# Kernel tuning notes

Measured on AMD Instinct MI355X. Metric: run time of the kernel, lower is better.

The kernel has to match this reference:

```python
import jax, jax.numpy as jnp
import numpy as np

C = 768
N = 2048
BS = 8
MASK_VAL = 1e10


def _sincos(n, c):
    # torch sinusoidal_position_embedding: interleaved sin/cos, then
    # cos_pos = emb[..., 1::2].repeat_interleave(2), sin_pos = emb[..., ::2].repeat_interleave(2)
    pos = jnp.arange(n, dtype=jnp.float32)[:, None]            # [N,1]
    inv = jnp.power(10000.0, -2.0 * jnp.arange(c // 2, dtype=jnp.float32) / c)  # [C/2]
    ang = pos * inv                                            # [N, C/2]
    sin = jnp.repeat(jnp.sin(ang), 2, axis=-1)                 # [N, C]
    cos = jnp.repeat(jnp.cos(ang), 2, axis=-1)                 # [N, C]
    return sin[None], cos[None]                                # [1, N, C]


def _rope(x, sin, cos):
    # x2 = interleave(-x_odd, x_even)
    x2 = jnp.stack([-x[..., 1::2], x[..., ::2]], axis=-1).reshape(x.shape)
    return x * cos + x2 * sin


def _global_pointer(x, Wq, bq, Wk, bk, sin, cos, mask):
    xq = jnp.einsum('bnc,dc->bnd', x, Wq) + bq
    xk = jnp.einsum('bnc,dc->bnd', x, Wk) + bk
    xq = _rope(xq, sin, cos)
    xk = _rope(xk, sin, cos)
    logits = jnp.einsum('bnd,bmd->bnm', xq, xk)
    logits = logits - mask * MASK_VAL
    return logits / jnp.sqrt(jnp.float32(C))


def setup_inputs() -> dict:
    key = jax.random.key(0)
    ks = jax.random.split(key, 9)
    s = 0.02
    return {
        'feature': jax.random.normal(ks[0], (BS, N, C), jnp.float32),
        'Wq': jax.random.normal(ks[1], (C, C), jnp.float32) * s,
        'bq': jax.random.normal(ks[2], (C,), jnp.float32) * s,
        'Wk': jax.random.normal(ks[3], (C, C), jnp.float32) * s,
        'bk': jax.random.normal(ks[4], (C,), jnp.float32) * s,
        'Wq_cls': jax.random.normal(ks[5], (C, C), jnp.float32) * s,
        'bq_cls': jax.random.normal(ks[6], (C,), jnp.float32) * s,
        'Wk_cls': jax.random.normal(ks[7], (C, C), jnp.float32) * s,
        'bk_cls': jax.random.normal(ks[8], (C,), jnp.float32) * s,
    }


def reference(feature, Wq, bq, Wk, bk, Wq_cls, bq_cls, Wk_cls, bk_cls):
    n = feature.shape[1]
    sin, cos = _sincos(n, C)
    mask = jnp.tril(jnp.ones((n, n), jnp.float32), k=-1)  # strictly lower triangular
    gp = _global_pointer(feature, Wq, bq, Wk, bk, sin, cos, mask)
    gp_cls = _global_pointer(feature, Wq_cls, bq_cls, Wk_cls, bk_cls, sin, cos, mask)
    # stacked: [2, bs, N, N] = (global_pointer, global_pointer_cls)
    return jnp.stack([gp, gp_cls], axis=0)
```

## Files before the change

### kernel.cpp

```cpp
#include <hip/hip_runtime.h>
#include <hip/hip_bf16.h>
#include <stdint.h>

typedef unsigned short u16;
typedef __attribute__((ext_vector_type(8))) __bf16 bf16x8;
typedef __attribute__((ext_vector_type(4))) float f32x4;

#define C_DIM 768
#define HALF_C 384
#define N_SEQ 2048
#define BATCH 8
#define M_TOT (BATCH * N_SEQ)
#define BK 32
#define NT (C_DIM / BK)

__device__ __forceinline__ u16 f2bf(float f) {
    union { float f; unsigned u; } c; c.f = f;
    unsigned r = (c.u + 0x7FFFu + ((c.u >> 16) & 1u)) >> 16;
    return (u16)r;
}

#define PREP_XBLK 12288
#define PREP_WBLK 576
#define PREP_SBLK 3072
__global__ __launch_bounds__(256) void prep_kernel(
    const float* __restrict__ feat,
    const float* __restrict__ Wq, const float* __restrict__ Wk,
    const float* __restrict__ Wqc, const float* __restrict__ Wkc,
    u16* __restrict__ xbf,
    u16* __restrict__ w0, u16* __restrict__ w1,
    u16* __restrict__ w2, u16* __restrict__ w3,
    uint32_t* __restrict__ cs_tab) {
    const int b = blockIdx.x, tid = threadIdx.x;
    if (b < PREP_XBLK + 4 * PREP_WBLK) {
        const float* src; u16* dst; int base;
        if (b < PREP_XBLK)                    { src = feat; dst = xbf; base = 0; }
        else if (b < PREP_XBLK + PREP_WBLK)   { src = Wq;  dst = w0; base = PREP_XBLK; }
        else if (b < PREP_XBLK + 2*PREP_WBLK) { src = Wk;  dst = w1; base = PREP_XBLK + PREP_WBLK; }
        else if (b < PREP_XBLK + 3*PREP_WBLK) { src = Wqc; dst = w2; base = PREP_XBLK + 2*PREP_WBLK; }
        else                                  { src = Wkc; dst = w3; base = PREP_XBLK + 3*PREP_WBLK; }
        const int i = (b - base) * 256 + tid;
        float4 v = ((const float4*)src)[i];
        ushort4 o;
        o.x = f2bf(v.x); o.y = f2bf(v.y); o.z = f2bf(v.z); o.w = f2bf(v.w);
        ((ushort4*)dst)[i] = o;
    } else {
        const int idx = (b - PREP_XBLK - 4 * PREP_WBLK) * 256 + tid;
        const int pos = idx / HALF_C;
        const int ip  = idx - pos * HALF_C;
        float inv = powf(10000.0f, (-2.0f / (float)C_DIM) * (float)ip);
        float ang = (float)pos * inv;
        uint32_t c = f2bf(cosf(ang)), s = f2bf(sinf(ang));
        cs_tab[idx] = (s << 16) | c;
    }
}

template<int N> __device__ __forceinline__ void vmwait();
template<> __device__ __forceinline__ void vmwait<8>() { asm volatile("s_waitcnt vmcnt(8)" ::: "memory"); }
template<> __device__ __forceinline__ void vmwait<4>() { asm volatile("s_waitcnt vmcnt(4)" ::: "memory"); }
template<> __device__ __forceinline__ void vmwait<0>() { asm volatile("s_waitcnt vmcnt(0)" ::: "memory"); }

__device__ __forceinline__ void async_load16(const void* src, void* dst_lds) {
    const __attribute__((address_space(1))) void* g =
        (const __attribute__((address_space(1))) void*)(uintptr_t)src;
    __attribute__((address_space(3))) void* l =
        (__attribute__((address_space(3))) void*)(unsigned)(uintptr_t)dst_lds;
    __builtin_amdgcn_global_load_lds(g, l, 16, 0, 0);
}

__device__ __forceinline__ void stage32(const u16* __restrict__ gbase, int ld,
                                        u16* ldsbase, int wave, int lane) {
    const int s  = (lane & 3) ^ ((lane >> 4) & 3);
    const int rr = lane >> 2;
    #pragma unroll
    for (int j = 0; j < 2; ++j) {
        const int chunk = wave * 2 + j;
        const u16* src = gbase + (size_t)(chunk * 16 + rr) * ld + s * 8;
        u16* dst = ldsbase + chunk * 512;
        async_load16(src, dst);
    }
}

__device__ __forceinline__ void gemm256_mainloop(
    const u16* __restrict__ A, const u16* __restrict__ B, int ld,
    u16* LdsA, u16* LdsB, f32x4 (&acc)[8][4], int wave, int lane) {

    #pragma unroll
    for (int t = 0; t < 3; ++t) {
        stage32(A + t * BK, ld, LdsA + t * 8192, wave, lane);
        stage32(B + t * BK, ld, LdsB + t * 8192, wave, lane);
    }
    __builtin_amdgcn_sched_barrier(0);
    vmwait<8>();
    __builtin_amdgcn_s_barrier();
    __builtin_amdgcn_sched_barrier(0);

    const int r = lane & 15, sl = lane >> 4;
    const int lane_off = r * 32 + ((sl ^ ((r >> 2) & 3)) * 8);
    const int wm = wave >> 2, wn = wave & 3;
    const int a_base = lane_off + wm * 512;
    const int b_base = lane_off + wn * 512;

    #pragma unroll
    for (int t = 0; t < NT; ++t) {
        const u16* At = LdsA + (t & 3) * 8192;
        const u16* Bt = LdsB + (t & 3) * 8192;
        bf16x8 a[4], b[4], a2[4];

        if (t + 3 < NT) stage32(A + (t + 3) * BK, ld, LdsA + ((t + 3) & 3) * 8192, wave, lane);
        #pragma unroll
        for (int mf = 0; mf < 4; ++mf) a[mf] = *(const bf16x8*)(At + a_base + mf * 1024);
        #pragma unroll
        for (int nf = 0; nf < 4; ++nf) b[nf] = *(const bf16x8*)(Bt + b_base + nf * 2048);
        __builtin_amdgcn_sched_barrier(0);
        __builtin_amdgcn_s_barrier();
        __builtin_amdgcn_sched_barrier(0);
        __builtin_amdgcn_s_setprio(1);
        #pragma unroll
        for (int mf = 0; mf < 4; ++mf)
            #pragma unroll
            for (int nf = 0; nf < 4; ++nf)
                acc[mf][nf] = __builtin_amdgcn_mfma_f32_16x16x32_bf16(a[mf], b[nf], acc[mf][nf], 0, 0, 0);
        __builtin_amdgcn_s_setprio(0);
        __builtin_amdgcn_sched_barrier(0);
        __builtin_amdgcn_s_barrier();
        __builtin_amdgcn_sched_barrier(0);

        if (t + 3 < NT) stage32(B + (t + 3) * BK, ld, LdsB + ((t + 3) & 3) * 8192, wave, lane);
        #pragma unroll
        for (int mf = 0; mf < 4; ++mf) a2[mf] = *(const bf16x8*)(At + a_base + (mf + 4) * 1024);
        __builtin_amdgcn_sched_barrier(0);
        __builtin_amdgcn_s_barrier();
        __builtin_amdgcn_sched_barrier(0);
        __builtin_amdgcn_s_setprio(1);
        #pragma unroll
        for (int mf = 0; mf < 4; ++mf)
            #pragma unroll
            for (int nf = 0; nf < 4; ++nf)
                acc[mf + 4][nf] = __builtin_amdgcn_mfma_f32_16x16x32_bf16(a2[mf], b[nf], acc[mf + 4][nf], 0, 0, 0);
        __builtin_amdgcn_s_setprio(0);
        __builtin_amdgcn_sched_barrier(0);
        if (t <= NT - 4)      vmwait<8>();
        else if (t == NT - 3) vmwait<4>();
        else if (t == NT - 2) vmwait<0>();
        __builtin_amdgcn_s_barrier();
        __builtin_amdgcn_sched_barrier(0);
    }
}

__global__ __launch_bounds__(512, 2) void proj_kernel(
    const u16* __restrict__ xbf,
    const u16* __restrict__ W0, const u16* __restrict__ W1,
    const u16* __restrict__ W2, const u16* __restrict__ W3,
    const float* __restrict__ b0, const float* __restrict__ b1,
    const float* __restrict__ b2, const float* __restrict__ b3,
    u16* __restrict__ o0, u16* __restrict__ o1, u16* __restrict__ o2, u16* __restrict__ o3,
    const uint32_t* __restrict__ cs_tab) {
    __shared__ __align__(16) u16 LdsA[4 * 8192];
    __shared__ __align__(16) u16 LdsB[4 * 8192];
    const int tid = threadIdx.x, lane = tid & 63, wave = tid >> 6;
    const int bid = blockIdx.x;
    const int swz = (bid & 7) * 96 + (bid >> 3);
    const int z   = swz / 192;
    const int rem = swz % 192;
    const int by  = rem / 64;
    const int bx  = rem % 64;
    const int m0 = bx * 256, n0 = by * 256;

    const u16*   W    = z == 0 ? W0 : z == 1 ? W1 : z == 2 ? W2 : W3;
    const float* bias = z == 0 ? b0 : z == 1 ? b1 : z == 2 ? b2 : b3;
    u16*         outp = z == 0 ? o0 : z == 1 ? o1 : z == 2 ? o2 : o3;

    f32x4 acc[8][4];
    #pragma unroll
    for (int x = 0; x < 8; ++x)
        #pragma unroll
        for (int y = 0; y < 4; ++y) acc[x][y] = f32x4{0.f, 0.f, 0.f, 0.f};

    gemm256_mainloop(xbf + (size_t)m0 * C_DIM, W + (size_t)n0 * C_DIM, C_DIM,
                     LdsA, LdsB, acc, wave, lane);

    const int wm = wave >> 2, wn = wave & 3;
    const int g = lane >> 4, r = lane & 15;
    #pragma unroll
    for (int nf = 0; nf < 4; ++nf) {
        const int col = n0 + nf * 64 + wn * 16 + r;
        const float bv = bias[col];
        const int ip = col >> 1;
        const float sgn = (col & 1) ? 1.0f : -1.0f;
        #pragma unroll
        for (int mf = 0; mf < 8; ++mf) {
            #pragma unroll
            for (int i = 0; i < 4; ++i) {
                const int row = m0 + mf * 32 + wm * 16 + g * 4 + i;
                const int pos = row & (N_SEQ - 1);
                float v = acc[mf][nf][i] + bv;
                float p = __shfl_xor(v, 1);
                const uint32_t cs = cs_tab[pos * HALF_C + ip];
                const float c = __uint_as_float(cs << 16);
                const float s = __uint_as_float(cs & 0xFFFF0000u);
                outp[(size_t)row * C_DIM + col] = f2bf(v * c + sgn * p * s);
            }
        }
    }
}

__global__ __launch_bounds__(512, 2) void logits_kernel(
    const u16* __restrict__ Q0, const u16* __restrict__ K0,
    const u16* __restrict__ Q1, const u16* __restrict__ K1,
    float* __restrict__ out) {
    __shared__ __align__(16) u16 LdsA[4 * 8192];
    __shared__ __align__(16) u16 LdsB[4 * 8192];
    const int tid = threadIdx.x, lane = tid & 63, wave = tid >> 6;
    const int bid = blockIdx.x;
    const int swz = (bid & 7) * 128 + (bid >> 3);
    const int z   = swz >> 6;
    const int rem = swz & 63;
    const int by  = rem >> 3;
    const int bx  = rem & 7;
    const int nrow0 = by * 256, mcol0 = bx * 256;

    const float RS = 0.036084391824351613f;
    const float MV = 1.0e10f * RS;
    float* outz = out + (size_t)z * N_SEQ * N_SEQ;

    if (bx < by) {
        const float4 cv = {-MV, -MV, -MV, -MV};
        #pragma unroll
        for (int i = 0; i < 32; ++i) {
            const int row = nrow0 + wave * 32 + i;
            *(float4*)(outz + (size_t)row * N_SEQ + mcol0 + lane * 4) = cv;
        }
        return;
    }

    const int h = z >> 3, b = z & 7;
    const u16* Qb = (h ? Q1 : Q0) + (size_t)b * N_SEQ * C_DIM;
    const u16* Kb = (h ? K1 : K0) + (size_t)b * N_SEQ * C_DIM;

    f32x4 acc[8][4];
    #pragma unroll
    for (int x = 0; x < 8; ++x)
        #pragma unroll
        for (int y = 0; y < 4; ++y) acc[x][y] = f32x4{0.f, 0.f, 0.f, 0.f};

    gemm256_mainloop(Qb + (size_t)nrow0 * C_DIM, Kb + (size_t)mcol0 * C_DIM, C_DIM,
                     LdsA, LdsB, acc, wave, lane);

    const int wm = wave >> 2, wn = wave & 3;
    const int g = lane >> 4, r = lane & 15;
    #pragma unroll
    for (int mf = 0; mf < 8; ++mf) {
        #pragma unroll
        for (int i = 0; i < 4; ++i) {
            const int row = nrow0 + mf * 32 + wm * 16 + g * 4 + i;
            float* orow = outz + (size_t)row * N_SEQ;
            #pragma unroll
            for (int nf = 0; nf < 4; ++nf) {
                const int col = mcol0 + nf * 64 + wn * 16 + r;
                orow[col] = acc[mf][nf][i] * RS - (col < row ? MV : 0.0f);
            }
        }
    }
}

extern "C" void kernel_launch(void* const* d_in, const int* in_sizes, int n_in,
                              void* d_out, int out_size, void* d_ws, size_t ws_size,
                              hipStream_t stream) {
    (void)in_sizes; (void)n_in; (void)out_size; (void)ws_size;
    const float* feat = (const float*)d_in[0];
    const float* Wq   = (const float*)d_in[1];
    const float* bq   = (const float*)d_in[2];
    const float* Wk   = (const float*)d_in[3];
    const float* bk   = (const float*)d_in[4];
    const float* Wqc  = (const float*)d_in[5];
    const float* bqc  = (const float*)d_in[6];
    const float* Wkc  = (const float*)d_in[7];
    const float* bkc  = (const float*)d_in[8];
    float* out = (float*)d_out;

    u16* ws = (u16*)d_ws;
    const size_t XE = (size_t)M_TOT * C_DIM;
    const size_t WE = (size_t)C_DIM * C_DIM;
    u16* xbf = ws;
    u16* Wb0 = ws + XE;
    u16* Wb1 = Wb0 + WE;
    u16* Wb2 = Wb1 + WE;
    u16* Wb3 = Wb2 + WE;
    u16* qkbase = Wb3 + WE;
    u16* Qa = qkbase;
    u16* Ka = qkbase + XE;
    u16* Qc = qkbase + 2 * XE;
    u16* Kc = qkbase + 3 * XE;
    uint32_t* cs_tab = (uint32_t*)(qkbase + 4 * XE);

    prep_kernel<<<dim3(PREP_XBLK + 4 * PREP_WBLK + PREP_SBLK), dim3(256), 0, stream>>>(
        feat, Wq, Wk, Wqc, Wkc, xbf, Wb0, Wb1, Wb2, Wb3, cs_tab);

    proj_kernel<<<dim3(768), dim3(512), 0, stream>>>(
        xbf, Wb0, Wb1, Wb2, Wb3, bq, bk, bqc, bkc, Qa, Ka, Qc, Kc, cs_tab);

    logits_kernel<<<dim3(1024), dim3(512), 0, stream>>>(
        Qa, Ka, Qc, Kc, out);
}
```

Baseline: 219.6 us.

## Shrink GEMM tiles to 128x256 with triple-buffered LDS and higher occupancy

Both GEMM kernels move from 256x256 tiles with a 4-stage split A/B LDS buffer to 128x256 tiles with a unified 3-stage buffer, and the per-iteration loop drops from two MFMA phases to one. Launch bounds rise to 4 blocks per CU and grid sizes double. The aim is more resident waves for latency hiding and finer-grained triangle skipping in the logits kernel. In exchange, each tile reuses operands less, the prefetch depth is shallower, and global traffic for the B operand goes up.

```diff
diff --git a/kernel.cpp b/kernel.cpp
--- a/kernel.cpp
+++ b/kernel.cpp
@@ -56,8 +56,7 @@
 }
 
 template<int N> __device__ __forceinline__ void vmwait();
-template<> __device__ __forceinline__ void vmwait<8>() { asm volatile("s_waitcnt vmcnt(8)" ::: "memory"); }
-template<> __device__ __forceinline__ void vmwait<4>() { asm volatile("s_waitcnt vmcnt(4)" ::: "memory"); }
+template<> __device__ __forceinline__ void vmwait<3>() { asm volatile("s_waitcnt vmcnt(3)" ::: "memory"); }
 template<> __device__ __forceinline__ void vmwait<0>() { asm volatile("s_waitcnt vmcnt(0)" ::: "memory"); }
 
 __device__ __forceinline__ void async_load16(const void* src, void* dst_lds) {
@@ -68,50 +67,51 @@
     __builtin_amdgcn_global_load_lds(g, l, 16, 0, 0);
 }
 
-__device__ __forceinline__ void stage32(const u16* __restrict__ gbase, int ld,
-                                        u16* ldsbase, int wave, int lane) {
+template<int NROWS>
+__device__ __forceinline__ void stageT(const u16* __restrict__ g, int ld,
+                                       u16* ldsbase, int wave, int lane) {
     const int s  = (lane & 3) ^ ((lane >> 4) & 3);
     const int rr = lane >> 2;
     #pragma unroll
-    for (int j = 0; j < 2; ++j) {
-        const int chunk = wave * 2 + j;
-        const u16* src = gbase + (size_t)(chunk * 16 + rr) * ld + s * 8;
-        u16* dst = ldsbase + chunk * 512;
-        async_load16(src, dst);
-    }
-}
-
-__device__ __forceinline__ void gemm256_mainloop(
+    for (int j = 0; j < NROWS / 128; ++j) {
+        const int chunk = wave + j * 8;
+        const u16* src = g + (size_t)(chunk * 16 + rr) * ld + s * 8;
+        async_load16(src, ldsbase + chunk * 512);
+    }
+}
+
+__device__ __forceinline__ void gemm_mainloop(
     const u16* __restrict__ A, const u16* __restrict__ B, int ld,
-    u16* LdsA, u16* LdsB, f32x4 (&acc)[8][4], int wave, int lane) {
-
-    #pragma unroll
-    for (int t = 0; t < 3; ++t) {
-        stage32(A + t * BK, ld, LdsA + t * 8192, wave, lane);
-        stage32(B + t * BK, ld, LdsB + t * 8192, wave, lane);
-    }
+    u16* Lds, f32x4 (&acc)[4][4], int wave, int lane) {
+
+    stageT<128>(A, ld, Lds, wave, lane);
+    stageT<256>(B, ld, Lds + 4096, wave, lane);
+    stageT<128>(A + BK, ld, Lds + 12288, wave, lane);
+    stageT<256>(B + BK, ld, Lds + 12288 + 4096, wave, lane);
     __builtin_amdgcn_sched_barrier(0);
-    vmwait<8>();
+    vmwait<3>();
     __builtin_amdgcn_s_barrier();
     __builtin_amdgcn_sched_barrier(0);
 
     const int r = lane & 15, sl = lane >> 4;
     const int lane_off = r * 32 + ((sl ^ ((r >> 2) & 3)) * 8);
     const int wm = wave >> 2, wn = wave & 3;
-    const int a_base = lane_off + wm * 512;
-    const int b_base = lane_off + wn * 512;
+    const int a_base = lane_off + wm * 2048;
+    const int b_base = 4096 + lane_off + wn * 2048;
 
     #pragma unroll
     for (int t = 0; t < NT; ++t) {
-        const u16* At = LdsA + (t & 3) * 8192;
-        const u16* Bt = LdsB + (t & 3) * 8192;
-        bf16x8 a[4], b[4], a2[4];
-
-        if (t + 3 < NT) stage32(A + (t + 3) * BK, ld, LdsA + ((t + 3) & 3) * 8192, wave, lane);
-        #pragma unroll
-        for (int mf = 0; mf < 4; ++mf) a[mf] = *(const bf16x8*)(At + a_base + mf * 1024);
-        #pragma unroll
-        for (int nf = 0; nf < 4; ++nf) b[nf] = *(const bf16x8*)(Bt + b_base + nf * 2048);
+        const u16* S = Lds + (t % 3) * 12288;
+        if (t + 2 < NT) {
+            u16* D = Lds + ((t + 2) % 3) * 12288;
+            stageT<128>(A + (t + 2) * BK, ld, D, wave, lane);
+            stageT<256>(B + (t + 2) * BK, ld, D + 4096, wave, lane);
+        }
+        bf16x8 a[4], b[4];
+        #pragma unroll
+        for (int mf = 0; mf < 4; ++mf) a[mf] = *(const bf16x8*)(S + a_base + mf * 512);
+        #pragma unroll
+        for (int nf = 0; nf < 4; ++nf) b[nf] = *(const bf16x8*)(S + b_base + nf * 512);
         __builtin_amdgcn_sched_barrier(0);
         __builtin_amdgcn_s_barrier();
         __builtin_amdgcn_sched_barrier(0);
@@ -123,32 +123,14 @@
                 acc[mf][nf] = __builtin_amdgcn_mfma_f32_16x16x32_bf16(a[mf], b[nf], acc[mf][nf], 0, 0, 0);
         __builtin_amdgcn_s_setprio(0);
         __builtin_amdgcn_sched_barrier(0);
-        __builtin_amdgcn_s_barrier();
-        __builtin_amdgcn_sched_barrier(0);
-
-        if (t + 3 < NT) stage32(B + (t + 3) * BK, ld, LdsB + ((t + 3) & 3) * 8192, wave, lane);
-        #pragma unroll
-        for (int mf = 0; mf < 4; ++mf) a2[mf] = *(const bf16x8*)(At + a_base + (mf + 4) * 1024);
-        __builtin_amdgcn_sched_barrier(0);
-        __builtin_amdgcn_s_barrier();
-        __builtin_amdgcn_sched_barrier(0);
-        __builtin_amdgcn_s_setprio(1);
-        #pragma unroll
-        for (int mf = 0; mf < 4; ++mf)
-            #pragma unroll
-            for (int nf = 0; nf < 4; ++nf)
-                acc[mf + 4][nf] = __builtin_amdgcn_mfma_f32_16x16x32_bf16(a2[mf], b[nf], acc[mf + 4][nf], 0, 0, 0);
-        __builtin_amdgcn_s_setprio(0);
-        __builtin_amdgcn_sched_barrier(0);
-        if (t <= NT - 4)      vmwait<8>();
-        else if (t == NT - 3) vmwait<4>();
+        if (t < NT - 2)       vmwait<3>();
         else if (t == NT - 2) vmwait<0>();
         __builtin_amdgcn_s_barrier();
         __builtin_amdgcn_sched_barrier(0);
     }
 }
 
-__global__ __launch_bounds__(512, 2) void proj_kernel(
+__global__ __launch_bounds__(512, 4) void proj_kernel(
     const u16* __restrict__ xbf,
     const u16* __restrict__ W0, const u16* __restrict__ W1,
     const u16* __restrict__ W2, const u16* __restrict__ W3,
@@ -156,43 +138,42 @@
     const float* __restrict__ b2, const float* __restrict__ b3,
     u16* __restrict__ o0, u16* __restrict__ o1, u16* __restrict__ o2, u16* __restrict__ o3,
     const uint32_t* __restrict__ cs_tab) {
-    __shared__ __align__(16) u16 LdsA[4 * 8192];
-    __shared__ __align__(16) u16 LdsB[4 * 8192];
+    __shared__ __align__(16) u16 Lds[3 * 12288];
     const int tid = threadIdx.x, lane = tid & 63, wave = tid >> 6;
     const int bid = blockIdx.x;
-    const int swz = (bid & 7) * 96 + (bid >> 3);
-    const int z   = swz / 192;
-    const int rem = swz % 192;
-    const int by  = rem / 64;
-    const int bx  = rem % 64;
-    const int m0 = bx * 256, n0 = by * 256;
+    const int swz = (bid & 7) * 192 + (bid >> 3);
+    const int z   = swz / 384;
+    const int rem = swz % 384;
+    const int by  = rem / 128;
+    const int bx  = rem % 128;
+    const int m0 = bx * 128, n0 = by * 256;
 
     const u16*   W    = z == 0 ? W0 : z == 1 ? W1 : z == 2 ? W2 : W3;
     const float* bias = z == 0 ? b0 : z == 1 ? b1 : z == 2 ? b2 : b3;
     u16*         outp = z == 0 ? o0 : z == 1 ? o1 : z == 2 ? o2 : o3;
 
-    f32x4 acc[8][4];
-    #pragma unroll
-    for (int x = 0; x < 8; ++x)
+    f32x4 acc[4][4];
+    #pragma unroll
+    for (int x = 0; x < 4; ++x)
         #pragma unroll
         for (int y = 0; y < 4; ++y) acc[x][y] = f32x4{0.f, 0.f, 0.f, 0.f};
 
-    gemm256_mainloop(xbf + (size_t)m0 * C_DIM, W + (size_t)n0 * C_DIM, C_DIM,
-                     LdsA, LdsB, acc, wave, lane);
+    gemm_mainloop(xbf + (size_t)m0 * C_DIM, W + (size_t)n0 * C_DIM, C_DIM,
+                  Lds, acc, wave, lane);
 
     const int wm = wave >> 2, wn = wave & 3;
     const int g = lane >> 4, r = lane & 15;
     #pragma unroll
     for (int nf = 0; nf < 4; ++nf) {
-        const int col = n0 + nf * 64 + wn * 16 + r;
+        const int col = n0 + wn * 64 + nf * 16 + r;
         const float bv = bias[col];
         const int ip = col >> 1;
         const float sgn = (col & 1) ? 1.0f : -1.0f;
         #pragma unroll
-        for (int mf = 0; mf < 8; ++mf) {
+        for (int mf = 0; mf < 4; ++mf) {
             #pragma unroll
             for (int i = 0; i < 4; ++i) {
-                const int row = m0 + mf * 32 + wm * 16 + g * 4 + i;
+                const int row = m0 + wm * 64 + mf * 16 + g * 4 + i;
                 const int pos = row & (N_SEQ - 1);
                 float v = acc[mf][nf][i] + bv;
                 float p = __shfl_xor(v, 1);
@@ -205,30 +186,29 @@
     }
 }
 
-__global__ __launch_bounds__(512, 2) void logits_kernel(
+__global__ __launch_bounds__(512, 4) void logits_kernel(
     const u16* __restrict__ Q0, const u16* __restrict__ K0,
     const u16* __restrict__ Q1, const u16* __restrict__ K1,
     float* __restrict__ out) {
-    __shared__ __align__(16) u16 LdsA[4 * 8192];
-    __shared__ __align__(16) u16 LdsB[4 * 8192];
+    __shared__ __align__(16) u16 Lds[3 * 12288];
     const int tid = threadIdx.x, lane = tid & 63, wave = tid >> 6;
     const int bid = blockIdx.x;
-    const int swz = (bid & 7) * 128 + (bid >> 3);
-    const int z   = swz >> 6;
-    const int rem = swz & 63;
+    const int swz = (bid & 7) * 256 + (bid >> 3);
+    const int z   = swz >> 7;
+    const int rem = swz & 127;
     const int by  = rem >> 3;
     const int bx  = rem & 7;
-    const int nrow0 = by * 256, mcol0 = bx * 256;
+    const int nrow0 = by * 128, mcol0 = bx * 256;
 
     const float RS = 0.036084391824351613f;
     const float MV = 1.0e10f * RS;
     float* outz = out + (size_t)z * N_SEQ * N_SEQ;
 
-    if (bx < by) {
+    if (mcol0 + 256 <= nrow0) {
         const float4 cv = {-MV, -MV, -MV, -MV};
         #pragma unroll
-        for (int i = 0; i < 32; ++i) {
-            const int row = nrow0 + wave * 32 + i;
+        for (int i = 0; i < 16; ++i) {
+            const int row = nrow0 + wave * 16 + i;
             *(float4*)(outz + (size_t)row * N_SEQ + mcol0 + lane * 4) = cv;
         }
         return;
@@ -238,26 +218,26 @@
     const u16* Qb = (h ? Q1 : Q0) + (size_t)b * N_SEQ * C_DIM;
     const u16* Kb = (h ? K1 : K0) + (size_t)b * N_SEQ * C_DIM;
 
-    f32x4 acc[8][4];
-    #pragma unroll
-    for (int x = 0; x < 8; ++x)
+    f32x4 acc[4][4];
+    #pragma unroll
+    for (int x = 0; x < 4; ++x)
         #pragma unroll
         for (int y = 0; y < 4; ++y) acc[x][y] = f32x4{0.f, 0.f, 0.f, 0.f};
 
-    gemm256_mainloop(Qb + (size_t)nrow0 * C_DIM, Kb + (size_t)mcol0 * C_DIM, C_DIM,
-                     LdsA, LdsB, acc, wave, lane);
+    gemm_mainloop(Qb + (size_t)nrow0 * C_DIM, Kb + (size_t)mcol0 * C_DIM, C_DIM,
+                  Lds, acc, wave, lane);
 
     const int wm = wave >> 2, wn = wave & 3;
     const int g = lane >> 4, r = lane & 15;
     #pragma unroll
-    for (int mf = 0; mf < 8; ++mf) {
+    for (int mf = 0; mf < 4; ++mf) {
         #pragma unroll
         for (int i = 0; i < 4; ++i) {
-            const int row = nrow0 + mf * 32 + wm * 16 + g * 4 + i;
+            const int row = nrow0 + wm * 64 + mf * 16 + g * 4 + i;
             float* orow = outz + (size_t)row * N_SEQ;
             #pragma unroll
             for (int nf = 0; nf < 4; ++nf) {
-                const int col = mcol0 + nf * 64 + wn * 16 + r;
+                const int col = mcol0 + wn * 64 + nf * 16 + r;
                 orow[col] = acc[mf][nf][i] * RS - (col < row ? MV : 0.0f);
             }
         }
@@ -297,9 +277,9 @@
     prep_kernel<<<dim3(PREP_XBLK + 4 * PREP_WBLK + PREP_SBLK), dim3(256), 0, stream>>>(
         feat, Wq, Wk, Wqc, Wkc, xbf, Wb0, Wb1, Wb2, Wb3, cs_tab);
 
-    proj_kernel<<<dim3(768), dim3(512), 0, stream>>>(
+    proj_kernel<<<dim3(1536), dim3(512), 0, stream>>>(
         xbf, Wb0, Wb1, Wb2, Wb3, bq, bk, bqc, bkc, Qa, Ka, Qc, Kc, cs_tab);
 
-    logits_kernel<<<dim3(1024), dim3(512), 0, stream>>>(
+    logits_kernel<<<dim3(2048), dim3(512), 0, stream>>>(
         Qa, Ka, Qc, Kc, out);
 }
```

Result: slower. 250.5 us (+14.1%).

## Make GEMM kernels persistent and prefetch the next tile across tile boundaries

Applied to the files above, without the earlier changes.

Both the projection and logits kernels now launch 256 persistent blocks. Each block loops over several 256x256 tiles assigned per XCD, and the async LDS prefetch of the next tile's first K-slices runs during the tail of the current tile, which hides the pipeline fill and drain at tile boundaries. The logits kernel now hands out only upper-triangle GEMM tiles to the loop and fills the masked lower tiles afterwards in a separate balanced pass. The wave-to-column mapping inside each tile also changes (wn*64+nf*16). The risks are load imbalance from tile counts of 2 or 3 per block, lower occupancy slack, and serialized epilogue stores inside the persistent loop.

```diff
diff --git a/kernel.cpp b/kernel.cpp
--- a/kernel.cpp
+++ b/kernel.cpp
@@ -68,85 +68,67 @@
     __builtin_amdgcn_global_load_lds(g, l, 16, 0, 0);
 }
 
-__device__ __forceinline__ void stage32(const u16* __restrict__ gbase, int ld,
+__device__ __forceinline__ void stage32(const u16* __restrict__ gbase,
                                         u16* ldsbase, int wave, int lane) {
     const int s  = (lane & 3) ^ ((lane >> 4) & 3);
     const int rr = lane >> 2;
     #pragma unroll
     for (int j = 0; j < 2; ++j) {
         const int chunk = wave * 2 + j;
-        const u16* src = gbase + (size_t)(chunk * 16 + rr) * ld + s * 8;
-        u16* dst = ldsbase + chunk * 512;
-        async_load16(src, dst);
-    }
-}
-
-__device__ __forceinline__ void gemm256_mainloop(
-    const u16* __restrict__ A, const u16* __restrict__ B, int ld,
-    u16* LdsA, u16* LdsB, f32x4 (&acc)[8][4], int wave, int lane) {
-
-    #pragma unroll
-    for (int t = 0; t < 3; ++t) {
-        stage32(A + t * BK, ld, LdsA + t * 8192, wave, lane);
-        stage32(B + t * BK, ld, LdsB + t * 8192, wave, lane);
-    }
-    __builtin_amdgcn_sched_barrier(0);
-    vmwait<8>();
-    __builtin_amdgcn_s_barrier();
-    __builtin_amdgcn_sched_barrier(0);
-
-    const int r = lane & 15, sl = lane >> 4;
-    const int lane_off = r * 32 + ((sl ^ ((r >> 2) & 3)) * 8);
-    const int wm = wave >> 2, wn = wave & 3;
-    const int a_base = lane_off + wm * 512;
-    const int b_base = lane_off + wn * 512;
-
-    #pragma unroll
-    for (int t = 0; t < NT; ++t) {
-        const u16* At = LdsA + (t & 3) * 8192;
-        const u16* Bt = LdsB + (t & 3) * 8192;
-        bf16x8 a[4], b[4], a2[4];
-
-        if (t + 3 < NT) stage32(A + (t + 3) * BK, ld, LdsA + ((t + 3) & 3) * 8192, wave, lane);
-        #pragma unroll
-        for (int mf = 0; mf < 4; ++mf) a[mf] = *(const bf16x8*)(At + a_base + mf * 1024);
-        #pragma unroll
-        for (int nf = 0; nf < 4; ++nf) b[nf] = *(const bf16x8*)(Bt + b_base + nf * 2048);
-        __builtin_amdgcn_sched_barrier(0);
-        __builtin_amdgcn_s_barrier();
-        __builtin_amdgcn_sched_barrier(0);
-        __builtin_amdgcn_s_setprio(1);
-        #pragma unroll
-        for (int mf = 0; mf < 4; ++mf)
-            #pragma unroll
-            for (int nf = 0; nf < 4; ++nf)
-                acc[mf][nf] = __builtin_amdgcn_mfma_f32_16x16x32_bf16(a[mf], b[nf], acc[mf][nf], 0, 0, 0);
-        __builtin_amdgcn_s_setprio(0);
-        __builtin_amdgcn_sched_barrier(0);
-        __builtin_amdgcn_s_barrier();
-        __builtin_amdgcn_sched_barrier(0);
-
-        if (t + 3 < NT) stage32(B + (t + 3) * BK, ld, LdsB + ((t + 3) & 3) * 8192, wave, lane);
-        #pragma unroll
-        for (int mf = 0; mf < 4; ++mf) a2[mf] = *(const bf16x8*)(At + a_base + (mf + 4) * 1024);
-        __builtin_amdgcn_sched_barrier(0);
-        __builtin_amdgcn_s_barrier();
-        __builtin_amdgcn_sched_barrier(0);
-        __builtin_amdgcn_s_setprio(1);
-        #pragma unroll
-        for (int mf = 0; mf < 4; ++mf)
-            #pragma unroll
-            for (int nf = 0; nf < 4; ++nf)
-                acc[mf + 4][nf] = __builtin_amdgcn_mfma_f32_16x16x32_bf16(a2[mf], b[nf], acc[mf + 4][nf], 0, 0, 0);
-        __builtin_amdgcn_s_setprio(0);
-        __builtin_amdgcn_sched_barrier(0);
-        if (t <= NT - 4)      vmwait<8>();
-        else if (t == NT - 3) vmwait<4>();
-        else if (t == NT - 2) vmwait<0>();
-        __builtin_amdgcn_s_barrier();
-        __builtin_amdgcn_sched_barrier(0);
-    }
-}
+        const u16* src = gbase + (size_t)(chunk * 16 + rr) * C_DIM + s * 8;
+        async_load16(src, ldsbase + chunk * 512);
+    }
+}
+
+#define GEMM_STREAM_TILE(Asp, Bsp, nA, nB, acc, last_tile)                            \
+    _Pragma("unroll")                                                                 \
+    for (int t = 0; t < NT; ++t) {                                                    \
+        const u16* At = LdsA + (t & 3) * 8192;                                        \
+        const u16* Bt = LdsB + (t & 3) * 8192;                                        \
+        u16* DA = LdsA + ((t + 3) & 3) * 8192;                                        \
+        u16* DB = LdsB + ((t + 3) & 3) * 8192;                                        \
+        const bool stage_on = !last_tile || (t < NT - 3);                             \
+        bf16x8 a[4], b[4], a2[4];                                                     \
+        if (stage_on) stage32(Asp, DA, wave, lane);                                   \
+        _Pragma("unroll")                                                             \
+        for (int mf = 0; mf < 4; ++mf) a[mf] = *(const bf16x8*)(At + a_base + mf * 1024); \
+        _Pragma("unroll")                                                             \
+        for (int nf = 0; nf < 4; ++nf) b[nf] = *(const bf16x8*)(Bt + b_base + nf * 2048); \
+        __builtin_amdgcn_sched_barrier(0);                                            \
+        __builtin_amdgcn_s_barrier();                                                 \
+        __builtin_amdgcn_sched_barrier(0);                                            \
+        __builtin_amdgcn_s_setprio(1);                                                \
+        _Pragma("unroll")                                                             \
+        for (int mf = 0; mf < 4; ++mf)                                                \
+            _Pragma("unroll")                                                         \
+            for (int nf = 0; nf < 4; ++nf)                                            \
+                acc[mf][nf] = __builtin_amdgcn_mfma_f32_16x16x32_bf16(a[mf], b[nf], acc[mf][nf], 0, 0, 0); \
+        __builtin_amdgcn_s_setprio(0);                                                \
+        __builtin_amdgcn_sched_barrier(0);                                            \
+        __builtin_amdgcn_s_barrier();                                                 \
+        __builtin_amdgcn_sched_barrier(0);                                            \
+        if (stage_on) stage32(Bsp, DB, wave, lane);                                   \
+        _Pragma("unroll")                                                             \
+        for (int mf = 0; mf < 4; ++mf) a2[mf] = *(const bf16x8*)(At + a_base + (mf + 4) * 1024); \
+        __builtin_amdgcn_sched_barrier(0);                                            \
+        __builtin_amdgcn_s_barrier();                                                 \
+        __builtin_amdgcn_sched_barrier(0);                                            \
+        __builtin_amdgcn_s_setprio(1);                                                \
+        _Pragma("unroll")                                                             \
+        for (int mf = 0; mf < 4; ++mf)                                                \
+            _Pragma("unroll")                                                         \
+            for (int nf = 0; nf < 4; ++nf)                                            \
+                acc[mf + 4][nf] = __builtin_amdgcn_mfma_f32_16x16x32_bf16(a2[mf], b[nf], acc[mf + 4][nf], 0, 0, 0); \
+        __builtin_amdgcn_s_setprio(0);                                                \
+        __builtin_amdgcn_sched_barrier(0);                                            \
+        if (t == NT - 4) { Asp = nA; Bsp = nB; } else { Asp += BK; Bsp += BK; }       \
+        if (t < NT - 3)       vmwait<8>();                                            \
+        else if (t == NT - 3) { if (last_tile) vmwait<4>(); else vmwait<8>(); }       \
+        else if (t == NT - 2) { if (last_tile) vmwait<0>(); else vmwait<8>(); }       \
+        else                  { if (!last_tile) vmwait<8>(); }                        \
+        __builtin_amdgcn_s_barrier();                                                 \
+        __builtin_amdgcn_sched_barrier(0);                                            \
+    }
 
 __global__ __launch_bounds__(512, 2) void proj_kernel(
     const u16* __restrict__ xbf,
@@ -159,47 +141,76 @@
     __shared__ __align__(16) u16 LdsA[4 * 8192];
     __shared__ __align__(16) u16 LdsB[4 * 8192];
     const int tid = threadIdx.x, lane = tid & 63, wave = tid >> 6;
-    const int bid = blockIdx.x;
-    const int swz = (bid & 7) * 96 + (bid >> 3);
-    const int z   = swz / 192;
-    const int rem = swz % 192;
-    const int by  = rem / 64;
-    const int bx  = rem % 64;
-    const int m0 = bx * 256, n0 = by * 256;
-
-    const u16*   W    = z == 0 ? W0 : z == 1 ? W1 : z == 2 ? W2 : W3;
-    const float* bias = z == 0 ? b0 : z == 1 ? b1 : z == 2 ? b2 : b3;
-    u16*         outp = z == 0 ? o0 : z == 1 ? o1 : z == 2 ? o2 : o3;
-
-    f32x4 acc[8][4];
+    const int xcd = blockIdx.x & 7, slot = blockIdx.x >> 3;
+    const int NTILE = 3;
+
+    auto decode = [&](int i, const u16*& A, const u16*& B, int& z, int& m0, int& n0) {
+        const int tile = xcd * 96 + slot + 32 * i;
+        z = tile / 192;
+        const int rem = tile - z * 192;
+        n0 = (rem >> 6) * 256;
+        m0 = (rem & 63) * 256;
+        const u16* W = z == 0 ? W0 : z == 1 ? W1 : z == 2 ? W2 : W3;
+        A = xbf + (size_t)m0 * C_DIM;
+        B = W + (size_t)n0 * C_DIM;
+    };
+
+    const int r = lane & 15, sl = lane >> 4;
+    const int lane_off = r * 32 + ((sl ^ ((r >> 2) & 3)) * 8);
+    const int wm = wave >> 2, wn = wave & 3;
+    const int a_base = lane_off + wm * 512;
+    const int b_base = lane_off + wn * 512;
+    const int g = lane >> 4;
+
+    const u16 *A0, *B0; int z0, m00, n00;
+    decode(0, A0, B0, z0, m00, n00);
     #pragma unroll
-    for (int x = 0; x < 8; ++x)
+    for (int k = 0; k < 3; ++k) {
+        stage32(A0 + k * BK, LdsA + k * 8192, wave, lane);
+        stage32(B0 + k * BK, LdsB + k * 8192, wave, lane);
+    }
+    __builtin_amdgcn_sched_barrier(0);
+    vmwait<8>();
+    __builtin_amdgcn_s_barrier();
+    __builtin_amdgcn_sched_barrier(0);
+    const u16 *Asp = A0 + 3 * BK, *Bsp = B0 + 3 * BK;
+
+    for (int ci = 0; ci < NTILE; ++ci) {
+        const u16 *Ac, *Bc; int z, m0, n0;
+        decode(ci, Ac, Bc, z, m0, n0);
+        const u16 *nA = Ac, *nB = Bc;
+        if (ci + 1 < NTILE) { int zz, mm, nn; decode(ci + 1, nA, nB, zz, mm, nn); }
+        const bool last = (ci == NTILE - 1);
+
+        f32x4 acc[8][4];
         #pragma unroll
-        for (int y = 0; y < 4; ++y) acc[x][y] = f32x4{0.f, 0.f, 0.f, 0.f};
-
-    gemm256_mainloop(xbf + (size_t)m0 * C_DIM, W + (size_t)n0 * C_DIM, C_DIM,
-                     LdsA, LdsB, acc, wave, lane);
-
-    const int wm = wave >> 2, wn = wave & 3;
-    const int g = lane >> 4, r = lane & 15;
-    #pragma unroll
-    for (int nf = 0; nf < 4; ++nf) {
-        const int col = n0 + nf * 64 + wn * 16 + r;
-        const float bv = bias[col];
-        const int ip = col >> 1;
-        const float sgn = (col & 1) ? 1.0f : -1.0f;
+        for (int x = 0; x < 8; ++x)
+            #pragma unroll
+            for (int y = 0; y < 4; ++y) acc[x][y] = f32x4{0.f, 0.f, 0.f, 0.f};
+
+        GEMM_STREAM_TILE(Asp, Bsp, nA, nB, acc, last)
+
+        const float* bias = z == 0 ? b0 : z == 1 ? b1 : z == 2 ? b2 : b3;
+        u16*         outp = z == 0 ? o0 : z == 1 ? o1 : z == 2 ? o2 : o3;
         #pragma unroll
-        for (int mf = 0; mf < 8; ++mf) {
-            #pragma unroll
-            for (int i = 0; i < 4; ++i) {
-                const int row = m0 + mf * 32 + wm * 16 + g * 4 + i;
-                const int pos = row & (N_SEQ - 1);
-                float v = acc[mf][nf][i] + bv;
-                float p = __shfl_xor(v, 1);
-                const uint32_t cs = cs_tab[pos * HALF_C + ip];
-                const float c = __uint_as_float(cs << 16);
-                const float s = __uint_as_float(cs & 0xFFFF0000u);
-                outp[(size_t)row * C_DIM + col] = f2bf(v * c + sgn * p * s);
+        for (int nf = 0; nf < 4; ++nf) {
+            const int col = n0 + wn * 64 + nf * 16 + r;
+            const float bv = bias[col];
+            const int ip = col >> 1;
+            const float sgn = (col & 1) ? 1.0f : -1.0f;
+            #pragma unroll
+            for (int mf = 0; mf < 8; ++mf) {
+                #pragma unroll
+                for (int i = 0; i < 4; ++i) {
+                    const int row = m0 + mf * 32 + wm * 16 + g * 4 + i;
+                    const int pos = row & (N_SEQ - 1);
+                    float v = acc[mf][nf][i] + bv;
+                    float p = __shfl_xor(v, 1);
+                    const uint32_t cs = cs_tab[pos * HALF_C + ip];
+                    const float c = __uint_as_float(cs << 16);
+                    const float s = __uint_as_float(cs & 0xFFFF0000u);
+                    outp[(size_t)row * C_DIM + col] = f2bf(v * c + sgn * p * s);
+                }
             }
         }
     }
@@ -212,53 +223,93 @@
     __shared__ __align__(16) u16 LdsA[4 * 8192];
     __shared__ __align__(16) u16 LdsB[4 * 8192];
     const int tid = threadIdx.x, lane = tid & 63, wave = tid >> 6;
-    const int bid = blockIdx.x;
-    const int swz = (bid & 7) * 128 + (bid >> 3);
-    const int z   = swz >> 6;
-    const int rem = swz & 63;
-    const int by  = rem >> 3;
-    const int bx  = rem & 7;
-    const int nrow0 = by * 256, mcol0 = bx * 256;
+    const int xcd = blockIdx.x & 7, slot = blockIdx.x >> 3;
+    const int ntile = (slot < 8) ? 3 : 2;
 
     const float RS = 0.036084391824351613f;
     const float MV = 1.0e10f * RS;
-    float* outz = out + (size_t)z * N_SEQ * N_SEQ;
-
-    if (bx < by) {
+
+    auto decode = [&](int i, const u16*& A, const u16*& B, int& z, int& nrow0, int& mcol0) {
+        const int c = xcd * 72 + slot + 32 * i;
+        z = c / 36;
+        int u = c - z * 36;
+        int by = 0;
+        while (u >= 8 - by) { u -= 8 - by; ++by; }
+        const int bx = by + u;
+        nrow0 = by * 256; mcol0 = bx * 256;
+        const int h = z >> 3, b = z & 7;
+        A = (h ? Q1 : Q0) + (size_t)b * N_SEQ * C_DIM + (size_t)nrow0 * C_DIM;
+        B = (h ? K1 : K0) + (size_t)b * N_SEQ * C_DIM + (size_t)mcol0 * C_DIM;
+    };
+
+    const int r = lane & 15, sl = lane >> 4;
+    const int lane_off = r * 32 + ((sl ^ ((r >> 2) & 3)) * 8);
+    const int wm = wave >> 2, wn = wave & 3;
+    const int a_base = lane_off + wm * 512;
+    const int b_base = lane_off + wn * 512;
+    const int g = lane >> 4;
+
+    const u16 *A0, *B0; int z0, nr0, mc0;
+    decode(0, A0, B0, z0, nr0, mc0);
+    #pragma unroll
+    for (int k = 0; k < 3; ++k) {
+        stage32(A0 + k * BK, LdsA + k * 8192, wave, lane);
+        stage32(B0 + k * BK, LdsB + k * 8192, wave, lane);
+    }
+    __builtin_amdgcn_sched_barrier(0);
+    vmwait<8>();
+    __builtin_amdgcn_s_barrier();
+    __builtin_amdgcn_sched_barrier(0);
+    const u16 *Asp = A0 + 3 * BK, *Bsp = B0 + 3 * BK;
+
+    for (int ci = 0; ci < ntile; ++ci) {
+        const u16 *Ac, *Bc; int z, nrow0, mcol0;
+        decode(ci, Ac, Bc, z, nrow0, mcol0);
+        const u16 *nA = Ac, *nB = Bc;
+        if (ci + 1 < ntile) { int zz, aa, bb; decode(ci + 1, nA, nB, zz, aa, bb); }
+        const bool last = (ci == ntile - 1);
+
+        f32x4 acc[8][4];
+        #pragma unroll
+        for (int x = 0; x < 8; ++x)
+            #pragma unroll
+            for (int y = 0; y < 4; ++y) acc[x][y] = f32x4{0.f, 0.f, 0.f, 0.f};
+
+        GEMM_STREAM_TILE(Asp, Bsp, nA, nB, acc, last)
+
+        float* outz = out + (size_t)z * N_SEQ * N_SEQ;
+        #pragma unroll
+        for (int mf = 0; mf < 8; ++mf) {
+            #pragma unroll
+            for (int i = 0; i < 4; ++i) {
+                const int row = nrow0 + mf * 32 + wm * 16 + g * 4 + i;
+                float* orow = outz + (size_t)row * N_SEQ;
+                #pragma unroll
+                for (int nf = 0; nf < 4; ++nf) {
+                    const int col = mcol0 + wn * 64 + nf * 16 + r;
+                    orow[col] = acc[mf][nf][i] * RS - (col < row ? MV : 0.0f);
+                }
+            }
+        }
+    }
+
+    if (slot >= 8) {
+        const int wl = slot - 8;
+        const int nw = (wl < 8) ? 3 : 2;
         const float4 cv = {-MV, -MV, -MV, -MV};
-        #pragma unroll
-        for (int i = 0; i < 32; ++i) {
-            const int row = nrow0 + wave * 32 + i;
-            *(float4*)(outz + (size_t)row * N_SEQ + mcol0 + lane * 4) = cv;
-        }
-        return;
-    }
-
-    const int h = z >> 3, b = z & 7;
-    const u16* Qb = (h ? Q1 : Q0) + (size_t)b * N_SEQ * C_DIM;
-    const u16* Kb = (h ? K1 : K0) + (size_t)b * N_SEQ * C_DIM;
-
-    f32x4 acc[8][4];
-    #pragma unroll
-    for (int x = 0; x < 8; ++x)
-        #pragma unroll
-        for (int y = 0; y < 4; ++y) acc[x][y] = f32x4{0.f, 0.f, 0.f, 0.f};
-
-    gemm256_mainloop(Qb + (size_t)nrow0 * C_DIM, Kb + (size_t)mcol0 * C_DIM, C_DIM,
-                     LdsA, LdsB, acc, wave, lane);
-
-    const int wm = wave >> 2, wn = wave & 3;
-    const int g = lane >> 4, r = lane & 15;
-    #pragma unroll
-    for (int mf = 0; mf < 8; ++mf) {
-        #pragma unroll
-        for (int i = 0; i < 4; ++i) {
-            const int row = nrow0 + mf * 32 + wm * 16 + g * 4 + i;
-            float* orow = outz + (size_t)row * N_SEQ;
-            #pragma unroll
-            for (int nf = 0; nf < 4; ++nf) {
-                const int col = mcol0 + nf * 64 + wn * 16 + r;
-                orow[col] = acc[mf][nf][i] * RS - (col < row ? MV : 0.0f);
+        for (int j = 0; j < nw; ++j) {
+            const int wid = xcd * 56 + wl + 24 * j;
+            const int z = wid / 28;
+            int l = wid - z * 28;
+            int by = 1;
+            while (l >= by) { l -= by; ++by; }
+            const int bx = l;
+            float* outz = out + (size_t)z * N_SEQ * N_SEQ;
+            const int nrow0 = by * 256, mcol0 = bx * 256;
+            #pragma unroll
+            for (int i = 0; i < 32; ++i) {
+                const int row = nrow0 + wave * 32 + i;
+                *(float4*)(outz + (size_t)row * N_SEQ + mcol0 + lane * 4) = cv;
             }
         }
     }
@@ -297,9 +348,9 @@
     prep_kernel<<<dim3(PREP_XBLK + 4 * PREP_WBLK + PREP_SBLK), dim3(256), 0, stream>>>(
         feat, Wq, Wk, Wqc, Wkc, xbf, Wb0, Wb1, Wb2, Wb3, cs_tab);
 
-    proj_kernel<<<dim3(768), dim3(512), 0, stream>>>(
+    proj_kernel<<<dim3(256), dim3(512), 0, stream>>>(
         xbf, Wb0, Wb1, Wb2, Wb3, bq, bk, bqc, bkc, Qa, Ka, Qc, Kc, cs_tab);
 
-    logits_kernel<<<dim3(1024), dim3(512), 0, stream>>>(
+    logits_kernel<<<dim3(256), dim3(512), 0, stream>>>(
         Qa, Ka, Qc, Kc, out);
 }
```

After: 325.5 us. 1.48x slower.
